# Kernel optimization log

Hardware: AMD Instinct MI355X
Metric: run time of the kernel (lower is better)

The kernel has to match this reference:

```python
import jax, jax.numpy as jnp
import numpy as np

ALPHA = 0.2  # LeakyReLU negative slope
NEG_INF = -1.0e12


def setup_inputs() -> dict:
    key = jax.random.key(0)
    k1, k2, k3, k4 = jax.random.split(key, 4)
    B, N, Fin, Fout = 4, 4096, 256, 128
    inp = jax.random.normal(k1, (B, N, Fin), dtype=jnp.float32)
    adj_weights = jax.random.uniform(k2, (B, N, N), dtype=jnp.float32)
    W = jax.random.normal(k3, (Fin, Fout), dtype=jnp.float32) * (1.414 / np.sqrt(Fin))
    a = jax.random.normal(k4, (2 * Fout, 1), dtype=jnp.float32) * 0.1
    return {"inp": inp, "adj_weights": adj_weights, "W": W, "a": a}


def reference(inp, adj_weights, W, a):
    Fout = W.shape[1]
    h = jnp.matmul(inp, W)                       # [B, N, Fout]
    # a_input[b,i,j] = concat(h[b,i], h[b,j]); matmul with a splits into two rank-1 terms
    a1 = a[:Fout, 0]                             # [Fout]
    a2 = a[Fout:, 0]                             # [Fout]
    s1 = jnp.einsum('bnf,f->bn', h, a1)          # [B, N]
    s2 = jnp.einsum('bnf,f->bn', h, a2)          # [B, N]
    e = jax.nn.leaky_relu(s1[:, :, None] + s2[:, None, :], negative_slope=ALPHA)  # [B,N,N]
    attention = jnp.where(adj_weights > 0, adj_weights * e, NEG_INF)
    attention = jax.nn.softmax(attention, axis=2)
    # dropout p=0.0 / eval mode -> identity
    h_prime = jnp.matmul(attention, h)           # [B, N, Fout]
    return jax.nn.elu(h_prime)                   # concat=True branch
```

## Files before the change

### kernel.cpp

```cpp
#include <hip/hip_runtime.h>
#include <math.h>

typedef float    float4_t __attribute__((ext_vector_type(4)));
typedef _Float16 half8    __attribute__((ext_vector_type(8)));

__global__ __launch_bounds__(256) void k_prep(const float* __restrict__ inp,
                                              const float* __restrict__ W,
                                              const float* __restrict__ a,
                                              float* __restrict__ s1,
                                              float* __restrict__ s2,
                                              _Float16* __restrict__ hT) {
    __shared__ float sA[32 * 68];
    __shared__ float sW[64 * 128];
    const int t   = threadIdx.x;
    const int gr0 = blockIdx.x * 32;
    const int b   = gr0 >> 12;
    const int f0  = (t & 15) * 8;
    const int r0  = (t >> 4) * 2;
    float4_t acc0[2] = {}; float4_t acc1[2] = {};
    for (int kc = 0; kc < 4; ++kc) {
        __syncthreads();
        #pragma unroll
        for (int it = 0; it < 2; ++it) {
            int fi = it * 256 + t; int r = fi >> 4; int c = (fi & 15) * 4;
            *(float4_t*)&sA[r * 68 + c] =
                *(const float4_t*)&inp[(size_t)(gr0 + r) * 256 + kc * 64 + c];
        }
        #pragma unroll
        for (int it = 0; it < 8; ++it) {
            int fi = it * 256 + t; int k = fi >> 5; int c = (fi & 31) * 4;
            *(float4_t*)&sW[k * 128 + c] =
                *(const float4_t*)&W[(size_t)(kc * 64 + k) * 128 + c];
        }
        __syncthreads();
        for (int k = 0; k < 64; ++k) {
            float4_t w0 = *(const float4_t*)&sW[k * 128 + f0];
            float4_t w1 = *(const float4_t*)&sW[k * 128 + f0 + 4];
            #pragma unroll
            for (int r = 0; r < 2; ++r) {
                float av = sA[(r0 + r) * 68 + k];
                acc0[r] += av * w0; acc1[r] += av * w1;
            }
        }
    }
    float4_t a1lo = *(const float4_t*)&a[f0];
    float4_t a1hi = *(const float4_t*)&a[f0 + 4];
    float4_t a2lo = *(const float4_t*)&a[128 + f0];
    float4_t a2hi = *(const float4_t*)&a[128 + f0 + 4];
    #pragma unroll
    for (int r = 0; r < 2; ++r) {
        const int row  = gr0 + r0 + r;
        const int rloc = row & 4095;
        #pragma unroll
        for (int c = 0; c < 4; ++c) {
            hT[(size_t)b * (128 * 4096) + (size_t)(f0 + c) * 4096 + rloc]     = (_Float16)acc0[r][c];
            hT[(size_t)b * (128 * 4096) + (size_t)(f0 + 4 + c) * 4096 + rloc] = (_Float16)acc1[r][c];
        }
        float p1 = acc0[r][0]*a1lo[0] + acc0[r][1]*a1lo[1] + acc0[r][2]*a1lo[2] + acc0[r][3]*a1lo[3]
                 + acc1[r][0]*a1hi[0] + acc1[r][1]*a1hi[1] + acc1[r][2]*a1hi[2] + acc1[r][3]*a1hi[3];
        float p2 = acc0[r][0]*a2lo[0] + acc0[r][1]*a2lo[1] + acc0[r][2]*a2lo[2] + acc0[r][3]*a2lo[3]
                 + acc1[r][0]*a2hi[0] + acc1[r][1]*a2hi[1] + acc1[r][2]*a2hi[2] + acc1[r][3]*a2hi[3];
        #pragma unroll
        for (int o = 1; o < 16; o <<= 1) { p1 += __shfl_xor(p1, o); p2 += __shfl_xor(p2, o); }
        if ((t & 15) == 0) { s1[row] = p1; s2[row] = p2; }
    }
}

__global__ __launch_bounds__(256) void k_s2max(const float* __restrict__ s2,
                                               float* __restrict__ s2max) {
    const int b = blockIdx.x, t = threadIdx.x;
    float m = -INFINITY;
    for (int i = t; i < 4096; i += 256) m = fmaxf(m, s2[b * 4096 + i]);
    #pragma unroll
    for (int o = 1; o < 64; o <<= 1) m = fmaxf(m, __shfl_xor(m, o));
    __shared__ float sm[4];
    if ((t & 63) == 0) sm[t >> 6] = m;
    __syncthreads();
    if (t == 0) s2max[b] = fmaxf(fmaxf(sm[0], sm[1]), fmaxf(sm[2], sm[3]));
}

__global__ __launch_bounds__(256, 4) void k_flash(const float* __restrict__ adj,
                                                  const _Float16* __restrict__ hT,
                                                  const float* __restrict__ s1,
                                                  const float* __restrict__ s2,
                                                  const float* __restrict__ s2max,
                                                  float* __restrict__ part_acc,
                                                  float* __restrict__ part_l) {
    __shared__ _Float16 hbuf[2][128 * 64];

    const int t    = threadIdx.x;
    const int bid  = blockIdx.x;
    const int sp   = bid & 3;
    const int rb   = (bid >> 2) & 63;
    const int b    = bid >> 8;
    const int w    = t >> 6, lane = t & 63;
    const int quad = lane >> 4, ln15 = lane & 15;
    const int rowb  = rb * 64 + w * 16;
    const int myrow = rowb + ln15;
    const float*    adj_r = adj + (size_t)b * 4096 * 4096 + (size_t)myrow * 4096;
    const _Float16* hT_b  = hT + (size_t)b * 128 * 4096;
    const float*    s2_b  = s2 + b * 4096;
    const float s1v  = s1[b * 4096 + myrow];
    const float mhat = fmaxf(0.f, s1v + s2max[b]);
    const int jwbase = sp * 1024;
    const int coff   = quad * 8;

    const int sf  = t >> 3;
    const int sc  = t & 7;
    const int fb7 = ln15 & 7;

    float4_t acc[8] = {};
    float psum = 0.f;

    float4_t adjc[4], adjn[4];
    #pragma unroll
    for (int kc = 0; kc < 2; ++kc) {
        adjc[kc * 2 + 0] = *(const float4_t*)&adj_r[jwbase + kc * 32 + coff];
        adjc[kc * 2 + 1] = *(const float4_t*)&adj_r[jwbase + kc * 32 + coff + 4];
    }
    {
        half8 hreg[4];
        #pragma unroll
        for (int i = 0; i < 4; ++i) {
            int f = i * 32 + sf;
            hreg[i] = *(const half8*)&hT_b[(size_t)f * 4096 + jwbase + sc * 8];
        }
        #pragma unroll
        for (int i = 0; i < 4; ++i) {
            int f = i * 32 + sf;
            *(half8*)&hbuf[0][f * 64 + ((sc ^ (f & 7)) << 3)] = hreg[i];
        }
    }
    __syncthreads();

    for (int jt = 0; jt < 16; ++jt) {
        const int cur = jt & 1;
        const int j0  = jwbase + jt * 64;
        half8 hreg[4];
        if (jt < 15) {
            #pragma unroll
            for (int i = 0; i < 4; ++i) {
                int f = i * 32 + sf;
                hreg[i] = *(const half8*)&hT_b[(size_t)f * 4096 + j0 + 64 + sc * 8];
            }
            #pragma unroll
            for (int kc = 0; kc < 2; ++kc) {
                adjn[kc * 2 + 0] = *(const float4_t*)&adj_r[j0 + 64 + kc * 32 + coff];
                adjn[kc * 2 + 1] = *(const float4_t*)&adj_r[j0 + 64 + kc * 32 + coff + 4];
            }
        }
        half8 afrag[2];
        #pragma unroll
        for (int kc = 0; kc < 2; ++kc) {
            #pragma unroll
            for (int hh = 0; hh < 2; ++hh) {
                float4_t sv = *(const float4_t*)&s2_b[j0 + kc * 32 + coff + hh * 4];
                float4_t av = adjc[kc * 2 + hh];
                #pragma unroll
                for (int c = 0; c < 4; ++c) {
                    float x = s1v + sv[c];
                    float e = x > 0.f ? x : 0.2f * x;
                    float p = av[c] > 0.f ? __expf(av[c] * e - mhat) : 0.f;
                    _Float16 q = (_Float16)p;
                    afrag[kc][hh * 4 + c] = q;
                    psum += (float)q;
                }
            }
        }
        #pragma unroll
        for (int nt = 0; nt < 8; ++nt) {
            #pragma unroll
            for (int kc = 0; kc < 2; ++kc) {
                const int fb = nt * 16 + ln15;
                half8 bfrag = *(const half8*)&hbuf[cur][fb * 64 + ((((kc << 2) + quad) ^ fb7) << 3)];
                acc[nt] = __builtin_amdgcn_mfma_f32_16x16x32_f16(afrag[kc], bfrag, acc[nt], 0, 0, 0);
            }
        }
        if (jt < 15) {
            #pragma unroll
            for (int i = 0; i < 4; ++i) {
                int f = i * 32 + sf;
                *(half8*)&hbuf[1 - cur][f * 64 + ((sc ^ (f & 7)) << 3)] = hreg[i];
            }
            #pragma unroll
            for (int q2 = 0; q2 < 4; ++q2) adjc[q2] = adjn[q2];
        }
        __syncthreads();
    }
    psum += __shfl_xor(psum, 16);
    psum += __shfl_xor(psum, 32);
    const size_t growb = (size_t)b * 4096 + rowb;
    if (lane < 16) part_l[(size_t)sp * 16384 + growb + lane] = psum;
    float* pacc = part_acc + (size_t)sp * 16384 * 128;
    #pragma unroll
    for (int nt = 0; nt < 8; ++nt) {
        #pragma unroll
        for (int reg = 0; reg < 4; ++reg) {
            pacc[(growb + quad * 4 + reg) * 128 + nt * 16 + ln15] = acc[nt][reg];
        }
    }
}

__global__ __launch_bounds__(256) void k_combine(const float* __restrict__ part_acc,
                                                 const float* __restrict__ part_l,
                                                 float* __restrict__ out) {
    const int idx = blockIdx.x * 256 + threadIdx.x;
    const int e0  = idx * 4;
    const int gr  = e0 >> 7;
    float l = part_l[gr] + part_l[16384 + gr] + part_l[32768 + gr] + part_l[49152 + gr];
    float4_t a0 = *(const float4_t*)&part_acc[e0];
    float4_t a1 = *(const float4_t*)&part_acc[2097152 + e0];
    float4_t a2 = *(const float4_t*)&part_acc[4194304 + e0];
    float4_t a3 = *(const float4_t*)&part_acc[6291456 + e0];
    float4_t s  = (a0 + a1) + (a2 + a3);
    float rl = 1.f / l;
    float4_t o;
    #pragma unroll
    for (int c = 0; c < 4; ++c) {
        float v = s[c] * rl;
        o[c] = v > 0.f ? v : expm1f(v);
    }
    *(float4_t*)&((float*)out)[e0] = o;
}

extern "C" void kernel_launch(void* const* d_in, const int* in_sizes, int n_in,
                              void* d_out, int out_size, void* d_ws, size_t ws_size,
                              hipStream_t stream) {
    const float* inp = (const float*)d_in[0];
    const float* adj = (const float*)d_in[1];
    const float* W   = (const float*)d_in[2];
    const float* a   = (const float*)d_in[3];
    float* out = (float*)d_out;

    char* wsb = (char*)d_ws;
    _Float16* hT       = (_Float16*)(wsb);
    float*    s1       = (float*)(wsb + 4194304);
    float*    s2       = (float*)(wsb + 4259840);
    float*    s2max    = (float*)(wsb + 4325376);
    float*    part_l   = (float*)(wsb + 4325632);
    float*    part_acc = (float*)(wsb + 4587776);

    hipLaunchKernelGGL(k_prep,    dim3(512),  dim3(256), 0, stream, inp, W, a, s1, s2, hT);
    hipLaunchKernelGGL(k_s2max,   dim3(4),    dim3(256), 0, stream, s2, s2max);
    hipLaunchKernelGGL(k_flash,   dim3(1024), dim3(256), 0, stream, adj, hT, s1, s2, s2max,
                       part_acc, part_l);
    hipLaunchKernelGGL(k_combine, dim3(2048), dim3(256), 0, stream, part_acc, part_l, out);
}
```

Baseline: 442.2 us.

## Coalesce adjacency loads and route probabilities through per-wave LDS tile

Each wave now reads the adjacency tile so that 16 lanes cover 64 contiguous columns of one row, instead of each lane reading 32-byte strips from its own row. This is meant to improve global-memory coalescing on the dominant 256 MB adjacency stream. The computed fp16 probabilities are written to a swizzled per-wave LDS buffer and read back in MFMA A-fragment layout, with row sums reduced by shuffles. The cost is extra LDS traffic and a waitcnt per tile, and the register prefetch of the next adjacency tile is dropped, so load latency is less hidden.

```diff
diff --git a/kernel.cpp b/kernel.cpp
--- a/kernel.cpp
+++ b/kernel.cpp
@@ -3,6 +3,7 @@
 
 typedef float    float4_t __attribute__((ext_vector_type(4)));
 typedef _Float16 half8    __attribute__((ext_vector_type(8)));
+typedef _Float16 half4_t  __attribute__((ext_vector_type(4)));
 
 __global__ __launch_bounds__(256) void k_prep(const float* __restrict__ inp,
                                               const float* __restrict__ W,
@@ -87,6 +88,7 @@
                                                   float* __restrict__ part_acc,
                                                   float* __restrict__ part_l) {
     __shared__ _Float16 hbuf[2][128 * 64];
+    __shared__ _Float16 pbuf[4][16 * 64];
 
     const int t    = threadIdx.x;
     const int bid  = blockIdx.x;
@@ -95,29 +97,29 @@
     const int b    = bid >> 8;
     const int w    = t >> 6, lane = t & 63;
     const int quad = lane >> 4, ln15 = lane & 15;
-    const int rowb  = rb * 64 + w * 16;
-    const int myrow = rowb + ln15;
-    const float*    adj_r = adj + (size_t)b * 4096 * 4096 + (size_t)myrow * 4096;
+    const int g    = quad;
+    const int cl   = ln15;
+    const int rowb = rb * 64 + w * 16;
+    const float*    adj_w = adj + (size_t)b * 4096 * 4096 + (size_t)rowb * 4096;
     const _Float16* hT_b  = hT + (size_t)b * 128 * 4096;
     const float*    s2_b  = s2 + b * 4096;
-    const float s1v  = s1[b * 4096 + myrow];
-    const float mhat = fmaxf(0.f, s1v + s2max[b]);
+    const float     s2m   = s2max[b];
     const int jwbase = sp * 1024;
-    const int coff   = quad * 8;
+
+    float s1r[4], mh[4];
+    #pragma unroll
+    for (int L = 0; L < 4; ++L) {
+        s1r[L] = s1[b * 4096 + rowb + L * 4 + g];
+        mh[L]  = fmaxf(0.f, s1r[L] + s2m);
+    }
 
     const int sf  = t >> 3;
     const int sc  = t & 7;
     const int fb7 = ln15 & 7;
 
     float4_t acc[8] = {};
-    float psum = 0.f;
-
-    float4_t adjc[4], adjn[4];
-    #pragma unroll
-    for (int kc = 0; kc < 2; ++kc) {
-        adjc[kc * 2 + 0] = *(const float4_t*)&adj_r[jwbase + kc * 32 + coff];
-        adjc[kc * 2 + 1] = *(const float4_t*)&adj_r[jwbase + kc * 32 + coff + 4];
-    }
+    float4_t psacc = {0.f, 0.f, 0.f, 0.f};
+
     {
         half8 hreg[4];
         #pragma unroll
@@ -143,29 +145,35 @@
                 int f = i * 32 + sf;
                 hreg[i] = *(const half8*)&hT_b[(size_t)f * 4096 + j0 + 64 + sc * 8];
             }
-            #pragma unroll
-            for (int kc = 0; kc < 2; ++kc) {
-                adjn[kc * 2 + 0] = *(const float4_t*)&adj_r[j0 + 64 + kc * 32 + coff];
-                adjn[kc * 2 + 1] = *(const float4_t*)&adj_r[j0 + 64 + kc * 32 + coff + 4];
-            }
-        }
+        }
+        float4_t av[4];
+        #pragma unroll
+        for (int L = 0; L < 4; ++L)
+            av[L] = *(const float4_t*)&adj_w[(size_t)(L * 4 + g) * 4096 + j0 + cl * 4];
+        float4_t s2v = *(const float4_t*)&s2_b[j0 + cl * 4];
+        #pragma unroll
+        for (int L = 0; L < 4; ++L) {
+            half4_t qv;
+            #pragma unroll
+            for (int c = 0; c < 4; ++c) {
+                float x = s1r[L] + s2v[c];
+                float e = x > 0.f ? x : 0.2f * x;
+                float p = av[L][c] > 0.f ? __expf(fmaf(av[L][c], e, -mh[L])) : 0.f;
+                _Float16 q = (_Float16)p;
+                qv[c] = q;
+                psacc[L] += (float)q;
+            }
+            const int r     = L * 4 + g;
+            const int c0    = cl * 4;
+            const int chunk = (c0 >> 3) ^ (r & 7);
+            *(half4_t*)&pbuf[w][r * 64 + chunk * 8 + (c0 & 7)] = qv;
+        }
+        asm volatile("s_waitcnt lgkmcnt(0)" ::: "memory");
         half8 afrag[2];
         #pragma unroll
         for (int kc = 0; kc < 2; ++kc) {
-            #pragma unroll
-            for (int hh = 0; hh < 2; ++hh) {
-                float4_t sv = *(const float4_t*)&s2_b[j0 + kc * 32 + coff + hh * 4];
-                float4_t av = adjc[kc * 2 + hh];
-                #pragma unroll
-                for (int c = 0; c < 4; ++c) {
-                    float x = s1v + sv[c];
-                    float e = x > 0.f ? x : 0.2f * x;
-                    float p = av[c] > 0.f ? __expf(av[c] * e - mhat) : 0.f;
-                    _Float16 q = (_Float16)p;
-                    afrag[kc][hh * 4 + c] = q;
-                    psum += (float)q;
-                }
-            }
+            const int chunk = ((kc << 2) + quad) ^ (ln15 & 7);
+            afrag[kc] = *(const half8*)&pbuf[w][ln15 * 64 + chunk * 8];
         }
         #pragma unroll
         for (int nt = 0; nt < 8; ++nt) {
@@ -182,15 +190,20 @@
                 int f = i * 32 + sf;
                 *(half8*)&hbuf[1 - cur][f * 64 + ((sc ^ (f & 7)) << 3)] = hreg[i];
             }
-            #pragma unroll
-            for (int q2 = 0; q2 < 4; ++q2) adjc[q2] = adjn[q2];
         }
         __syncthreads();
     }
-    psum += __shfl_xor(psum, 16);
-    psum += __shfl_xor(psum, 32);
+    #pragma unroll
+    for (int o = 1; o < 16; o <<= 1) {
+        #pragma unroll
+        for (int L = 0; L < 4; ++L) psacc[L] += __shfl_xor(psacc[L], o);
+    }
     const size_t growb = (size_t)b * 4096 + rowb;
-    if (lane < 16) part_l[(size_t)sp * 16384 + growb + lane] = psum;
+    if (cl == 0) {
+        #pragma unroll
+        for (int L = 0; L < 4; ++L)
+            part_l[(size_t)sp * 16384 + growb + L * 4 + g] = psacc[L];
+    }
     float* pacc = part_acc + (size_t)sp * 16384 * 128;
     #pragma unroll
     for (int nt = 0; nt < 8; ++nt) {
```

After: 432.6 us. 2.2% less time.
